# Performance work log

Measured on AMD Instinct MI355X. Metric: run time of the kernel, lower is better.

The kernel has to match this reference:

```python
import jax, jax.numpy as jnp
import numpy as np

N_HEADS = 32
N_KV = 8
HEAD_DIM = 128
THETA = 1000000.0


def setup_inputs() -> dict:
    key = jax.random.key(0)
    ks = jax.random.split(key, 7)
    batch, q_len, history = 4, 1024, 1024
    T = batch * q_len
    H = N_HEADS * HEAD_DIM  # 4096
    kv_len = q_len + history
    block_size = 64
    num_blocks = batch * (kv_len // block_size)  # 128
    s = 0.02
    return {
        'hidden_states': jax.random.normal(ks[0], (T, H), jnp.float32),
        'wq': jax.random.normal(ks[1], (H, N_HEADS * HEAD_DIM), jnp.float32) * s,
        'wk': jax.random.normal(ks[2], (H, N_KV * HEAD_DIM), jnp.float32) * s,
        'wv': jax.random.normal(ks[3], (H, N_KV * HEAD_DIM), jnp.float32) * s,
        'wo': jax.random.normal(ks[4], (N_HEADS * HEAD_DIM, H), jnp.float32) * s,
        'k_cache': jax.random.normal(ks[5], (num_blocks, block_size, N_KV, HEAD_DIM), jnp.float32),
        'v_cache': jax.random.normal(ks[6], (num_blocks, block_size, N_KV, HEAD_DIM), jnp.float32),
        'q_len': q_len,
        'history': history,
        'window': 1024,
    }


def _rotate_half(x):
    d = x.shape[-1]
    return jnp.concatenate([-x[..., d // 2:], x[..., :d // 2]], axis=-1)


def reference(hidden_states, wq, wk, wv, wo, k_cache, v_cache, q_len, history, window):
    T, H = hidden_states.shape
    batch = T // q_len
    kv_len = q_len + history
    nb, bs, n_kv, d = k_cache.shape
    blocks_per_seq = kv_len // bs
    # block table: sequence b owns contiguous blocks (paged layout)
    block_offsets = jnp.arange(batch * blocks_per_seq).reshape(batch, blocks_per_seq)

    # QKV projections
    q = (hidden_states @ wq).reshape(T, N_HEADS, d)
    k = (hidden_states @ wk).reshape(T, n_kv, d)
    v = (hidden_states @ wv).reshape(T, n_kv, d)

    # RoPE using 1d position ids (global positions of new tokens)
    pos = jnp.broadcast_to(history + jnp.arange(q_len), (batch, q_len)).reshape(T)
    inv_freq = 1.0 / (THETA ** (jnp.arange(0, d, 2, dtype=jnp.float32) / d))
    freqs = pos[:, None].astype(jnp.float32) * inv_freq[None, :]
    emb = jnp.concatenate([freqs, freqs], axis=-1)  # [T, d]
    cos = jnp.cos(emb)[:, None, :].astype(q.dtype)
    sin = jnp.sin(emb)[:, None, :].astype(q.dtype)
    q = q * cos + _rotate_half(q) * sin
    k = k * cos + _rotate_half(k) * sin

    # fill_kv_cache: scatter new K/V into paged slots history..kv_len-1
    new_pos = history + jnp.arange(q_len)  # [q_len]
    slot = (block_offsets[:, new_pos // bs] * bs + new_pos % bs).reshape(T)
    k_flat = k_cache.reshape(nb * bs, n_kv, d).at[slot].set(k)
    v_flat = v_cache.reshape(nb * bs, n_kv, d).at[slot].set(v)

    # paged gather of the full KV window per sequence
    all_pos = jnp.arange(kv_len)
    gslot = block_offsets[:, all_pos // bs] * bs + all_pos % bs  # [batch, kv_len]
    k_all = k_flat[gslot]  # [batch, kv_len, n_kv, d]
    v_all = v_flat[gslot]

    # GQA: expand kv heads
    rep = N_HEADS // n_kv
    k_all = jnp.repeat(k_all, rep, axis=2)
    v_all = jnp.repeat(v_all, rep, axis=2)

    qb = q.reshape(batch, q_len, N_HEADS, d)
    scores = jnp.einsum('bqhd,bkhd->bhqk', qb, k_all) / jnp.sqrt(jnp.asarray(d, qb.dtype))

    # causal + sliding-window mask on global positions
    qpos = history + jnp.arange(q_len)
    kpos = jnp.arange(kv_len)
    mask = kpos[None, :] <= qpos[:, None]
    if window > 0:
        mask = mask & ((qpos[:, None] - kpos[None, :]) < window)
    neg = jnp.finfo(scores.dtype).min
    scores = jnp.where(mask[None, None], scores, neg)
    attn = jax.nn.softmax(scores, axis=-1)
    out = jnp.einsum('bhqk,bkhd->bqhd', attn, v_all).reshape(T, N_HEADS * d)
    return out @ wo
```

## Files before the change

kernel.cpp:

```cpp
#include <hip/hip_runtime.h>
#include <hip/hip_bf16.h>

typedef __bf16 bf16x8 __attribute__((ext_vector_type(8)));
typedef __bf16 bf16x4 __attribute__((ext_vector_type(4)));
typedef float  f32x4  __attribute__((ext_vector_type(4)));

#define QL 1024
#define NH 32
#define NKV 8
#define HD 128
#define KVLEN 2048
#define QKV_LD 6144

typedef const __attribute__((address_space(1))) void gv_t;
typedef __attribute__((address_space(3))) void lv_t;
__device__ __forceinline__ void gll16(const void* g, void* l) {
  __builtin_amdgcn_global_load_lds((gv_t*)g, (lv_t*)l, 16, 0, 0);
}

__global__ __launch_bounds__(256) void cast_plain(const float* __restrict__ in,
                                                  __bf16* __restrict__ out, int n4) {
  int i = blockIdx.x * 256 + threadIdx.x;
  if (i >= n4) return;
  float4 v = ((const float4*)in)[i];
  bf16x4 o;
  o[0] = (__bf16)v.x; o[1] = (__bf16)v.y; o[2] = (__bf16)v.z; o[3] = (__bf16)v.w;
  ((bf16x4*)out)[i] = o;
}

__global__ __launch_bounds__(256) void transpose_cast(const float* __restrict__ in,
                                                      __bf16* __restrict__ out,
                                                      int R, int C) {
  __shared__ __bf16 tile[64][65];
  int r0 = blockIdx.y * 64, c0 = blockIdx.x * 64;
  int t = threadIdx.x;
  int tr = t >> 4, tc = (t & 15) * 4;
#pragma unroll
  for (int pass = 0; pass < 4; pass++) {
    int r = pass * 16 + tr;
    float4 v = *(const float4*)(in + (size_t)(r0 + r) * C + c0 + tc);
    tile[r][tc + 0] = (__bf16)v.x;
    tile[r][tc + 1] = (__bf16)v.y;
    tile[r][tc + 2] = (__bf16)v.z;
    tile[r][tc + 3] = (__bf16)v.w;
  }
  __syncthreads();
#pragma unroll
  for (int pass = 0; pass < 4; pass++) {
    int cc = pass * 16 + tr;
    bf16x4 o;
#pragma unroll
    for (int j = 0; j < 4; j++) o[j] = tile[tc + j][cc];
    *(bf16x4*)(out + (size_t)(c0 + cc) * R + r0 + tc) = o;
  }
}

template <int OUT_BF16>
__global__ __launch_bounds__(512, 2) void gemm256(const __bf16* __restrict__ A,
                                                  const __bf16* __restrict__ Bt,
                                                  void* __restrict__ Cout,
                                                  int M, int N, int K) {
  __shared__ __attribute__((aligned(16))) __bf16 sA[4][8192];
  __shared__ __attribute__((aligned(16))) __bf16 sB[4][8192];
  const int tid = threadIdx.x;
  const int lane = tid & 63;
  const int wave = tid >> 6;
  const int wm = wave >> 2, wn = wave & 3;
  const int quad = lane >> 4, l16 = lane & 15;

  const int nwg = gridDim.x;
  const int id = blockIdx.x;
  const int swz = (id & 7) * (nwg >> 3) + (id >> 3);
  const int gx = N >> 8;
  const int by = swz / gx, bx = swz - by * gx;
  const int row0 = by * 256, col0 = bx * 256;

  const int qsel = (tid & 3) ^ ((tid >> 3) & 3);
  const __bf16* pA0 = A + (size_t)(row0 + (tid >> 2)) * K + qsel * 8;
  const __bf16* pA1 = pA0 + (size_t)128 * K;
  const __bf16* pB0 = Bt + (size_t)(col0 + (tid >> 2)) * K + qsel * 8;
  const __bf16* pB1 = pB0 + (size_t)128 * K;

  const int xsw = (l16 >> 1) & 3;
  const int aoff = (wm * 128 + l16) * 32 + (quad ^ xsw) * 8;
  const int boff = (wn * 64 + l16) * 32 + (quad ^ xsw) * 8;

  f32x4 acc[8][4];
#pragma unroll
  for (int mt = 0; mt < 8; mt++)
#pragma unroll
    for (int nt = 0; nt < 4; nt++) acc[mt][nt] = (f32x4){0.f, 0.f, 0.f, 0.f};

  const int nT = K >> 5;

  for (int pt = 0; pt < 3; ++pt) {
    __bf16* dA = &sA[pt][0];
    __bf16* dB = &sB[pt][0];
    gll16(pA0, dA + tid * 8);
    gll16(pA1, dA + 4096 + tid * 8);
    gll16(pB0, dB + tid * 8);
    gll16(pB1, dB + 4096 + tid * 8);
    pA0 += 32; pA1 += 32; pB0 += 32; pB1 += 32;
  }
  asm volatile("s_waitcnt vmcnt(8)" ::: "memory");
  __builtin_amdgcn_s_barrier();

  for (int t = 0; t < nT; ++t) {
    const int bt = t & 3;
    const bool st = (t + 3 < nT);
    const __bf16* Ab = &sA[bt][aoff];
    const __bf16* Bb = &sB[bt][boff];
    __bf16* dA = &sA[(t + 3) & 3][0];
    __bf16* dB = &sB[(t + 3) & 3][0];
    bf16x8 a[4], b[4];

#pragma unroll
    for (int i = 0; i < 4; ++i) a[i] = *(const bf16x8*)(Ab + i * 512);
#pragma unroll
    for (int i = 0; i < 4; ++i) b[i] = *(const bf16x8*)(Bb + i * 512);
    if (st) {
      gll16(pA0, dA + tid * 8);
      gll16(pA1, dA + 4096 + tid * 8);
    }
    asm volatile("" ::: "memory");
    __builtin_amdgcn_s_barrier();
    __builtin_amdgcn_s_setprio(1);
#pragma unroll
    for (int mt = 0; mt < 4; ++mt)
#pragma unroll
      for (int nt = 0; nt < 4; ++nt)
        acc[mt][nt] = __builtin_amdgcn_mfma_f32_16x16x32_bf16(a[mt], b[nt], acc[mt][nt], 0, 0, 0);
    __builtin_amdgcn_s_setprio(0);
    __builtin_amdgcn_s_barrier();

#pragma unroll
    for (int i = 0; i < 4; ++i) a[i] = *(const bf16x8*)(Ab + (4 + i) * 512);
    if (st) {
      gll16(pB0, dB + tid * 8);
      gll16(pB1, dB + 4096 + tid * 8);
      pA0 += 32; pA1 += 32; pB0 += 32; pB1 += 32;
    }
    if (t + 3 < nT) {
      asm volatile("s_waitcnt vmcnt(8)" ::: "memory");
    } else if (t + 2 < nT) {
      asm volatile("s_waitcnt vmcnt(4)" ::: "memory");
    } else if (t + 1 < nT) {
      asm volatile("s_waitcnt vmcnt(0)" ::: "memory");
    }
    __builtin_amdgcn_s_barrier();
    __builtin_amdgcn_s_setprio(1);
#pragma unroll
    for (int mt = 0; mt < 4; ++mt)
#pragma unroll
      for (int nt = 0; nt < 4; ++nt)
        acc[4 + mt][nt] = __builtin_amdgcn_mfma_f32_16x16x32_bf16(a[mt], b[nt], acc[4 + mt][nt], 0, 0, 0);
    __builtin_amdgcn_s_setprio(0);
    __builtin_amdgcn_s_barrier();
  }

#pragma unroll
  for (int mt = 0; mt < 8; ++mt) {
#pragma unroll
    for (int r = 0; r < 4; ++r) {
      const int grow = row0 + wm * 128 + mt * 16 + quad * 4 + r;
#pragma unroll
      for (int nt = 0; nt < 4; ++nt) {
        const int gcol = col0 + wn * 64 + nt * 16 + l16;
        float v = acc[mt][nt][r];
        if (OUT_BF16)
          ((__bf16*)Cout)[(size_t)grow * N + gcol] = (__bf16)v;
        else
          ((float*)Cout)[(size_t)grow * N + gcol] = v;
      }
    }
  }
}

__global__ __launch_bounds__(256) void rope_kernel(__bf16* __restrict__ qkv) {
  int idx = blockIdx.x * 256 + threadIdx.x;
  int m = idx & 63;
  int rest = idx >> 6;
  int t = rest / 40;
  int head = rest - t * 40;
  int i = t & (QL - 1);
  float pos = (float)(1024 + i);
  float ang = pos * exp2f(-(float)m * 0.31143075889569403f);
  float c = cosf(ang), sn = sinf(ang);
  size_t base = (size_t)t * QKV_LD + head * HD;
  float x0 = (float)qkv[base + m];
  float x1 = (float)qkv[base + 64 + m];
  qkv[base + m]      = (__bf16)(x0 * c - x1 * sn);
  qkv[base + 64 + m] = (__bf16)(x1 * c + x0 * sn);
}

__global__ __launch_bounds__(256) void kv_build_k(const float* __restrict__ kcache,
                                                  const __bf16* __restrict__ qkv,
                                                  __bf16* __restrict__ k_all) {
  int idx = blockIdx.x * 256 + threadIdx.x;
  int d8 = (idx & 15) * 8;
  int p = (idx >> 4) & (KVLEN - 1);
  int bk = idx >> 15;
  int b = bk >> 3, kvh = bk & 7;
  __bf16* dst = k_all + ((size_t)bk * KVLEN + p) * HD + d8;
  if (p < 1024) {
    const float* src = kcache + ((size_t)(b * KVLEN + p) * NKV + kvh) * HD + d8;
    bf16x8 o;
#pragma unroll
    for (int j = 0; j < 8; j++) o[j] = (__bf16)src[j];
    *(bf16x8*)dst = o;
  } else {
    const __bf16* src = qkv + (size_t)(b * QL + p - 1024) * QKV_LD + 4096 + kvh * HD + d8;
    *(bf16x8*)dst = *(const bf16x8*)src;
  }
}

__global__ __launch_bounds__(256) void kv_build_vT(const float* __restrict__ vcache,
                                                   const __bf16* __restrict__ qkv,
                                                   __bf16* __restrict__ v_allT) {
  __shared__ __bf16 tile[64][130];
  int blk = blockIdx.x;
  int pt = blk & 31, bk = blk >> 5;
  int b = bk >> 3, kvh = bk & 7;
  int p0 = pt * 64;
  int t = threadIdx.x;
  int lr = t >> 4, d8 = (t & 15) * 8;
#pragma unroll
  for (int pass = 0; pass < 4; pass++) {
    int pl = pass * 16 + lr;
    int p = p0 + pl;
    if (p < 1024) {
      const float* src = vcache + ((size_t)(b * KVLEN + p) * NKV + kvh) * HD + d8;
#pragma unroll
      for (int j = 0; j < 8; j++) tile[pl][d8 + j] = (__bf16)src[j];
    } else {
      const __bf16* src = qkv + (size_t)(b * QL + p - 1024) * QKV_LD + 5120 + kvh * HD + d8;
      bf16x8 v = *(const bf16x8*)src;
#pragma unroll
      for (int j = 0; j < 8; j++) tile[pl][d8 + j] = v[j];
    }
  }
  __syncthreads();
#pragma unroll
  for (int pass = 0; pass < 4; pass++) {
    int d = (t >> 3) + pass * 32;
    int ps = (t & 7) * 8;
    bf16x8 o;
#pragma unroll
    for (int j = 0; j < 8; j++) o[j] = tile[ps + j][d];
    *(bf16x8*)(v_allT + ((size_t)bk * HD + d) * KVLEN + p0 + ps) = o;
  }
}

__global__ __launch_bounds__(256) void attn_kernel(const __bf16* __restrict__ qkv,
                                                   const __bf16* __restrict__ k_all,
                                                   const __bf16* __restrict__ v_allT,
                                                   __bf16* __restrict__ out) {
  __shared__ __attribute__((aligned(16))) __bf16 sK[64 * 128];
  __shared__ __attribute__((aligned(16))) __bf16 sV[128 * 64];
  __shared__ __attribute__((aligned(16))) __bf16 sP[4][32 * 72];
  const int tid = threadIdx.x;
  const int lane = tid & 63;
  const int wave = tid >> 6;
  const int quad = lane >> 4, l16 = lane & 15;
  const int bid = blockIdx.x;
  const int b = bid & 3;
  const int kvh = (bid >> 2) & 7;
  const int qt = bid >> 5;
  const int h = kvh * 4 + wave;
  const int i0 = qt * 32;

  const __bf16* kb = k_all + (size_t)(b * NKV + kvh) * KVLEN * HD;
  const __bf16* vb = v_allT + (size_t)(b * NKV + kvh) * HD * KVLEN;

  bf16x8 qf[2][4];
#pragma unroll
  for (int mt = 0; mt < 2; mt++) {
    const __bf16* qb = qkv + (size_t)(b * QL + i0 + mt * 16 + l16) * QKV_LD + h * HD + quad * 8;
#pragma unroll
    for (int kc = 0; kc < 4; kc++) qf[mt][kc] = *(const bf16x8*)(qb + kc * 32);
  }

  int kgo[4], vgo[4];
#pragma unroll
  for (int j = 0; j < 4; j++) {
    int g = wave * 4 + j;
    kgo[j] = (g * 4 + quad) * HD + (l16 ^ (g & 7)) * 8;
    int d = g * 8 + (lane >> 3);
    vgo[j] = d * KVLEN + ((lane & 7) ^ ((lane >> 3) & 7)) * 8;
  }
  __bf16* kls = sK + (wave * 4) * 512 + lane * 8;
  __bf16* vls = sV + (wave * 4) * 512 + lane * 8;

  f32x4 o[8][2];
#pragma unroll
  for (int dt = 0; dt < 8; dt++)
#pragma unroll
    for (int mt = 0; mt < 2; mt++) o[dt][mt] = (f32x4){0.f, 0.f, 0.f, 0.f};
  f32x4 lac[2];
  lac[0] = (f32x4){0.f, 0.f, 0.f, 0.f};
  lac[1] = (f32x4){0.f, 0.f, 0.f, 0.f};

  bf16x8 ones;
#pragma unroll
  for (int j = 0; j < 8; j++) ones[j] = (__bf16)1.0f;

  __bf16* myP = &sP[wave][0];
  const float ES = 0.12751744f;

  const int cs = (i0 + 1) & ~63;
  const int xsw = l16 & 7;

#pragma unroll
  for (int j = 0; j < 4; j++) gll16(kb + (size_t)cs * HD + kgo[j], kls + j * 512);
#pragma unroll
  for (int j = 0; j < 4; j++) gll16(vb + (size_t)cs + vgo[j], vls + j * 512);

  for (int ci = 0; ci < 17; ci++) {
    const int c = cs + ci * 64;
    __syncthreads();
    f32x4 s[2][4];
#pragma unroll
    for (int nt = 0; nt < 4; nt++) {
      s[0][nt] = (f32x4){0.f, 0.f, 0.f, 0.f};
      s[1][nt] = (f32x4){0.f, 0.f, 0.f, 0.f};
      const __bf16* kp = sK + (4 * l16 + nt) * HD;
#pragma unroll
      for (int kc = 0; kc < 4; kc++) {
        bf16x8 kf = *(const bf16x8*)(kp + ((4 * kc + quad) ^ xsw) * 8);
        s[0][nt] = __builtin_amdgcn_mfma_f32_16x16x32_bf16(qf[0][kc], kf, s[0][nt], 0, 0, 0);
        s[1][nt] = __builtin_amdgcn_mfma_f32_16x16x32_bf16(qf[1][kc], kf, s[1][nt], 0, 0, 0);
      }
    }
    __syncthreads();
    if (ci < 16) {
#pragma unroll
      for (int j = 0; j < 4; j++) gll16(kb + (size_t)(c + 64) * HD + kgo[j], kls + j * 512);
    }
    const bool full = (c >= i0 + 32) && (c <= i0 + 961);
#pragma unroll
    for (int mt = 0; mt < 2; mt++) {
#pragma unroll
      for (int r = 0; r < 4; r++) {
        bf16x4 pk;
        if (full) {
#pragma unroll
          for (int nt = 0; nt < 4; nt++) pk[nt] = (__bf16)exp2f(s[mt][nt][r] * ES);
        } else {
          const int irow = i0 + mt * 16 + quad * 4 + r;
#pragma unroll
          for (int nt = 0; nt < 4; nt++) {
            const int kk = c + 4 * l16 + nt;
            const bool valid = (kk > irow) && (kk <= irow + 1024);
            pk[nt] = valid ? (__bf16)exp2f(s[mt][nt][r] * ES) : (__bf16)0.0f;
          }
        }
        *(bf16x4*)(myP + (mt * 16 + quad * 4 + r) * 72 + 4 * l16) = pk;
      }
    }
    asm volatile("s_waitcnt lgkmcnt(0)" ::: "memory");
#pragma unroll
    for (int kc = 0; kc < 2; kc++) {
      bf16x8 pf0 = *(const bf16x8*)(myP + (l16) * 72 + kc * 32 + quad * 8);
      bf16x8 pf1 = *(const bf16x8*)(myP + (16 + l16) * 72 + kc * 32 + quad * 8);
      lac[0] = __builtin_amdgcn_mfma_f32_16x16x32_bf16(pf0, ones, lac[0], 0, 0, 0);
      lac[1] = __builtin_amdgcn_mfma_f32_16x16x32_bf16(pf1, ones, lac[1], 0, 0, 0);
#pragma unroll
      for (int dt = 0; dt < 8; dt++) {
        bf16x8 vf = *(const bf16x8*)(sV + (dt * 16 + l16) * 64 + ((kc * 4 + quad) ^ xsw) * 8);
        o[dt][0] = __builtin_amdgcn_mfma_f32_16x16x32_bf16(pf0, vf, o[dt][0], 0, 0, 0);
        o[dt][1] = __builtin_amdgcn_mfma_f32_16x16x32_bf16(pf1, vf, o[dt][1], 0, 0, 0);
      }
    }
    __syncthreads();
    if (ci < 16) {
#pragma unroll
      for (int j = 0; j < 4; j++) gll16(vb + (size_t)(c + 64) + vgo[j], vls + j * 512);
    }
  }

  float inv[2][4];
#pragma unroll
  for (int mt = 0; mt < 2; mt++)
#pragma unroll
    for (int r = 0; r < 4; r++) inv[mt][r] = 1.0f / lac[mt][r];
#pragma unroll
  for (int dt = 0; dt < 8; dt++)
#pragma unroll
    for (int mt = 0; mt < 2; mt++)
#pragma unroll
      for (int r = 0; r < 4; r++)
        out[(size_t)(b * QL + i0 + mt * 16 + quad * 4 + r) * (NH * HD) + h * HD + dt * 16 + l16] =
            (__bf16)(o[dt][mt][r] * inv[mt][r]);
}

extern "C" void kernel_launch(void* const* d_in, const int* in_sizes, int n_in,
                              void* d_out, int out_size, void* d_ws, size_t ws_size,
                              hipStream_t stream) {
  const float* hidden = (const float*)d_in[0];
  const float* wq = (const float*)d_in[1];
  const float* wk = (const float*)d_in[2];
  const float* wv = (const float*)d_in[3];
  const float* wo = (const float*)d_in[4];
  const float* kcache = (const float*)d_in[5];
  const float* vcache = (const float*)d_in[6];
  (void)in_sizes; (void)n_in; (void)out_size; (void)ws_size;

  char* w = (char*)d_ws;
  __bf16* hid_b  = (__bf16*)(w);
  __bf16* wqkvT  = (__bf16*)(w + 33554432ULL);
  __bf16* qkv    = (__bf16*)(w + 83886080ULL);
  __bf16* k_all  = (__bf16*)(w + 134217728ULL);
  __bf16* v_allT = (__bf16*)(w + 150994944ULL);
  __bf16* attn   = hid_b;
  __bf16* woT    = wqkvT;

  cast_plain<<<16384, 256, 0, stream>>>(hidden, hid_b, 4194304);
  transpose_cast<<<dim3(64, 64), 256, 0, stream>>>(wq, wqkvT, 4096, 4096);
  transpose_cast<<<dim3(16, 64), 256, 0, stream>>>(wk, wqkvT + 16777216ULL, 4096, 1024);
  transpose_cast<<<dim3(16, 64), 256, 0, stream>>>(wv, wqkvT + 20971520ULL, 4096, 1024);
  gemm256<1><<<dim3(384), 512, 0, stream>>>(hid_b, wqkvT, (void*)qkv, 4096, 6144, 4096);
  rope_kernel<<<40960, 256, 0, stream>>>(qkv);
  kv_build_k<<<4096, 256, 0, stream>>>(kcache, qkv, k_all);
  kv_build_vT<<<1024, 256, 0, stream>>>(vcache, qkv, v_allT);
  attn_kernel<<<1024, 256, 0, stream>>>(qkv, k_all, v_allT, attn);
  transpose_cast<<<dim3(64, 64), 256, 0, stream>>>(wo, woT, 4096, 4096);
  gemm256<0><<<dim3(256), 512, 0, stream>>>(attn, woT, d_out, 4096, 4096, 4096);
}
```

Measured before the change: 773.9 us.

## Switch GEMMs to 128x256 tiles with double-buffered 64-wide K stages

Replaces the 256x256 GEMM tile with a 128x256 tile using 64-wide K steps split into two halves, double-buffered in LDS instead of a 4-deep 32-wide ring. It doubles the grid (768 and 512 workgroups) to fill more of the 256 CUs and better balance the tail wave. It also adds serpentine ordering of column tiles on odd rows for L2 reuse. The trade-offs are lower arithmetic intensity per tile and a shallower prefetch pipeline.

```diff
diff --git a/kernel.cpp b/kernel.cpp
--- a/kernel.cpp
+++ b/kernel.cpp
@@ -56,12 +56,12 @@
 }
 
 template <int OUT_BF16>
-__global__ __launch_bounds__(512, 2) void gemm256(const __bf16* __restrict__ A,
-                                                  const __bf16* __restrict__ Bt,
-                                                  void* __restrict__ Cout,
-                                                  int M, int N, int K) {
-  __shared__ __attribute__((aligned(16))) __bf16 sA[4][8192];
-  __shared__ __attribute__((aligned(16))) __bf16 sB[4][8192];
+__global__ __launch_bounds__(512, 2) void gemm128x256(const __bf16* __restrict__ A,
+                                                      const __bf16* __restrict__ Bt,
+                                                      void* __restrict__ Cout,
+                                                      int M, int N, int K) {
+  __shared__ __attribute__((aligned(16))) __bf16 sA[2][8192];
+  __shared__ __attribute__((aligned(16))) __bf16 sB[2][16384];
   const int tid = threadIdx.x;
   const int lane = tid & 63;
   const int wave = tid >> 6;
@@ -70,82 +70,80 @@
 
   const int nwg = gridDim.x;
   const int id = blockIdx.x;
-  const int swz = (id & 7) * (nwg >> 3) + (id >> 3);
+  int swz = (id & 7) * (nwg >> 3) + (id >> 3);
   const int gx = N >> 8;
-  const int by = swz / gx, bx = swz - by * gx;
-  const int row0 = by * 256, col0 = bx * 256;
+  int by = swz / gx;
+  int bx = swz - by * gx;
+  if (by & 1) bx = gx - 1 - bx;
+  const int row0 = by * 128, col0 = bx * 256;
 
   const int qsel = (tid & 3) ^ ((tid >> 3) & 3);
-  const __bf16* pA0 = A + (size_t)(row0 + (tid >> 2)) * K + qsel * 8;
-  const __bf16* pA1 = pA0 + (size_t)128 * K;
-  const __bf16* pB0 = Bt + (size_t)(col0 + (tid >> 2)) * K + qsel * 8;
-  const __bf16* pB1 = pB0 + (size_t)128 * K;
-
-  const int xsw = (l16 >> 1) & 3;
-  const int aoff = (wm * 128 + l16) * 32 + (quad ^ xsw) * 8;
-  const int boff = (wn * 64 + l16) * 32 + (quad ^ xsw) * 8;
-
-  f32x4 acc[8][4];
-#pragma unroll
-  for (int mt = 0; mt < 8; mt++)
+  const __bf16* gA  = A  + (size_t)(row0 + (tid >> 2)) * K + qsel * 8;
+  const __bf16* gB0 = Bt + (size_t)(col0 + (tid >> 2)) * K + qsel * 8;
+  const __bf16* gB1 = gB0 + (size_t)128 * K;
+
+  const int xq = (quad ^ ((l16 >> 1) & 3)) * 8;
+  const int abase = (wm * 64 + l16) * 32 + xq;
+  const int bbase = (wn * 64 + l16) * 32 + xq;
+
+  f32x4 acc[4][4];
+#pragma unroll
+  for (int mt = 0; mt < 4; mt++)
 #pragma unroll
     for (int nt = 0; nt < 4; nt++) acc[mt][nt] = (f32x4){0.f, 0.f, 0.f, 0.f};
 
-  const int nT = K >> 5;
-
-  for (int pt = 0; pt < 3; ++pt) {
-    __bf16* dA = &sA[pt][0];
-    __bf16* dB = &sB[pt][0];
-    gll16(pA0, dA + tid * 8);
-    gll16(pA1, dA + 4096 + tid * 8);
-    gll16(pB0, dB + tid * 8);
-    gll16(pB1, dB + 4096 + tid * 8);
-    pA0 += 32; pA1 += 32; pB0 += 32; pB1 += 32;
-  }
-  asm volatile("s_waitcnt vmcnt(8)" ::: "memory");
+  const int nT = K >> 6;
+
+#define STAGE_A(t_, kh_)                                                        \
+  gll16(gA + (size_t)(t_)*64 + (kh_)*32, &sA[(t_) & 1][(kh_)*4096] + tid * 8)
+#define STAGE_B(t_, kh_)                                                        \
+  do {                                                                          \
+    __bf16* d_ = &sB[(t_) & 1][(kh_)*8192];                                     \
+    gll16(gB0 + (size_t)(t_)*64 + (kh_)*32, d_ + tid * 8);                      \
+    gll16(gB1 + (size_t)(t_)*64 + (kh_)*32, d_ + 4096 + tid * 8);               \
+  } while (0)
+
+  STAGE_A(0, 0); STAGE_B(0, 0);
+  STAGE_A(0, 1); STAGE_B(0, 1);
+  if (nT > 1) { STAGE_A(1, 0); STAGE_B(1, 0); }
+  asm volatile("s_waitcnt vmcnt(6)" ::: "memory");
   __builtin_amdgcn_s_barrier();
 
   for (int t = 0; t < nT; ++t) {
-    const int bt = t & 3;
-    const bool st = (t + 3 < nT);
-    const __bf16* Ab = &sA[bt][aoff];
-    const __bf16* Bb = &sB[bt][boff];
-    __bf16* dA = &sA[(t + 3) & 3][0];
-    __bf16* dB = &sB[(t + 3) & 3][0];
-    bf16x8 a[4], b[4];
-
-#pragma unroll
-    for (int i = 0; i < 4; ++i) a[i] = *(const bf16x8*)(Ab + i * 512);
-#pragma unroll
-    for (int i = 0; i < 4; ++i) b[i] = *(const bf16x8*)(Bb + i * 512);
-    if (st) {
-      gll16(pA0, dA + tid * 8);
-      gll16(pA1, dA + 4096 + tid * 8);
-    }
-    asm volatile("" ::: "memory");
+    const __bf16* Ab = &sA[t & 1][0];
+    const __bf16* Bb = &sB[t & 1][0];
+    bf16x8 af[4], bfr[4];
+
+#pragma unroll
+    for (int i = 0; i < 4; ++i) af[i]  = *(const bf16x8*)(Ab + abase + i * 512);
+#pragma unroll
+    for (int i = 0; i < 4; ++i) bfr[i] = *(const bf16x8*)(Bb + bbase + i * 512);
+    if (t + 1 < nT) {
+      STAGE_A(t + 1, 1); STAGE_B(t + 1, 1);
+      asm volatile("s_waitcnt vmcnt(6)" ::: "memory");
+    } else {
+      asm volatile("s_waitcnt vmcnt(0)" ::: "memory");
+    }
     __builtin_amdgcn_s_barrier();
     __builtin_amdgcn_s_setprio(1);
 #pragma unroll
     for (int mt = 0; mt < 4; ++mt)
 #pragma unroll
       for (int nt = 0; nt < 4; ++nt)
-        acc[mt][nt] = __builtin_amdgcn_mfma_f32_16x16x32_bf16(a[mt], b[nt], acc[mt][nt], 0, 0, 0);
+        acc[mt][nt] = __builtin_amdgcn_mfma_f32_16x16x32_bf16(af[mt], bfr[nt], acc[mt][nt], 0, 0, 0);
     __builtin_amdgcn_s_setprio(0);
-    __builtin_amdgcn_s_barrier();
-
-#pragma unroll
-    for (int i = 0; i < 4; ++i) a[i] = *(const bf16x8*)(Ab + (4 + i) * 512);
-    if (st) {
-      gll16(pB0, dB + tid * 8);
-      gll16(pB1, dB + 4096 + tid * 8);
-      pA0 += 32; pA1 += 32; pB0 += 32; pB1 += 32;
-    }
-    if (t + 3 < nT) {
-      asm volatile("s_waitcnt vmcnt(8)" ::: "memory");
-    } else if (t + 2 < nT) {
-      asm volatile("s_waitcnt vmcnt(4)" ::: "memory");
+
+#pragma unroll
+    for (int i = 0; i < 4; ++i) af[i]  = *(const bf16x8*)(Ab + 4096 + abase + i * 512);
+#pragma unroll
+    for (int i = 0; i < 4; ++i) bfr[i] = *(const bf16x8*)(Bb + 8192 + bbase + i * 512);
+    if (t + 2 < nT) {
+      STAGE_A(t + 2, 0); STAGE_B(t + 2, 0);
+      asm volatile("s_waitcnt vmcnt(6)" ::: "memory");
     } else if (t + 1 < nT) {
-      asm volatile("s_waitcnt vmcnt(0)" ::: "memory");
+      asm volatile("s_waitcnt vmcnt(3)" ::: "memory");
+    } else {
+      asm volatile("" ::: "memory");
     }
     __builtin_amdgcn_s_barrier();
     __builtin_amdgcn_s_setprio(1);
@@ -153,16 +151,17 @@
     for (int mt = 0; mt < 4; ++mt)
 #pragma unroll
       for (int nt = 0; nt < 4; ++nt)
-        acc[4 + mt][nt] = __builtin_amdgcn_mfma_f32_16x16x32_bf16(a[mt], b[nt], acc[4 + mt][nt], 0, 0, 0);
+        acc[mt][nt] = __builtin_amdgcn_mfma_f32_16x16x32_bf16(af[mt], bfr[nt], acc[mt][nt], 0, 0, 0);
     __builtin_amdgcn_s_setprio(0);
-    __builtin_amdgcn_s_barrier();
-  }
-
-#pragma unroll
-  for (int mt = 0; mt < 8; ++mt) {
+  }
+#undef STAGE_A
+#undef STAGE_B
+
+#pragma unroll
+  for (int mt = 0; mt < 4; ++mt) {
 #pragma unroll
     for (int r = 0; r < 4; ++r) {
-      const int grow = row0 + wm * 128 + mt * 16 + quad * 4 + r;
+      const int grow = row0 + wm * 64 + mt * 16 + quad * 4 + r;
 #pragma unroll
       for (int nt = 0; nt < 4; ++nt) {
         const int gcol = col0 + wn * 64 + nt * 16 + l16;
@@ -418,11 +417,11 @@
   transpose_cast<<<dim3(64, 64), 256, 0, stream>>>(wq, wqkvT, 4096, 4096);
   transpose_cast<<<dim3(16, 64), 256, 0, stream>>>(wk, wqkvT + 16777216ULL, 4096, 1024);
   transpose_cast<<<dim3(16, 64), 256, 0, stream>>>(wv, wqkvT + 20971520ULL, 4096, 1024);
-  gemm256<1><<<dim3(384), 512, 0, stream>>>(hid_b, wqkvT, (void*)qkv, 4096, 6144, 4096);
+  gemm128x256<1><<<dim3(768), 512, 0, stream>>>(hid_b, wqkvT, (void*)qkv, 4096, 6144, 4096);
   rope_kernel<<<40960, 256, 0, stream>>>(qkv);
   kv_build_k<<<4096, 256, 0, stream>>>(kcache, qkv, k_all);
   kv_build_vT<<<1024, 256, 0, stream>>>(vcache, qkv, v_allT);
   attn_kernel<<<1024, 256, 0, stream>>>(qkv, k_all, v_allT, attn);
   transpose_cast<<<dim3(64, 64), 256, 0, stream>>>(wo, woT, 4096, 4096);
-  gemm256<0><<<dim3(256), 512, 0, stream>>>(attn, woT, d_out, 4096, 4096, 4096);
-}
+  gemm128x256<0><<<dim3(512), 512, 0, stream>>>(attn, woT, d_out, 4096, 4096, 4096);
+}
```

Measured after the change: 802.9 us. 3.7% more time.

## Add 128x256-tile GEMM for QKV projection and restructure RoPE per token

Applied to the files above, without the earlier changes.

Adds a new bf16 MFMA GEMM kernel with 128x256 tiles, double-buffered LDS staging through global_load_lds, an XOR-swizzled LDS layout, priority hints, and launch bounds that allow two blocks per CU. The QKV projection switches to it with 768 workgroups instead of 384, aiming for more waves on the device and better tail balance. The RoPE kernel now gives one block per token and loops over the 40 heads, so cos/sin are computed once per thread rather than once per element. The cost is less reuse per tile, since each block covers half as many rows as before.

```diff
diff --git a/kernel.cpp b/kernel.cpp
--- a/kernel.cpp
+++ b/kernel.cpp
@@ -176,21 +176,145 @@
   }
 }
 
+template <int OUT_BF16>
+__global__ __launch_bounds__(512, 2) void gemm128x256(const __bf16* __restrict__ A,
+                                                      const __bf16* __restrict__ Bt,
+                                                      void* __restrict__ Cout,
+                                                      int M, int N, int K) {
+  __shared__ __attribute__((aligned(16))) __bf16 sA[2][8192];
+  __shared__ __attribute__((aligned(16))) __bf16 sB[2][16384];
+  const int tid = threadIdx.x;
+  const int lane = tid & 63;
+  const int wave = tid >> 6;
+  const int wm = wave >> 2, wn = wave & 3;
+  const int quad = lane >> 4, l16 = lane & 15;
+
+  const int nwg = gridDim.x;
+  const int id = blockIdx.x;
+  int swz = (id & 7) * (nwg >> 3) + (id >> 3);
+  const int gx = N >> 8;
+  int by = swz / gx;
+  int bx = swz - by * gx;
+  if (by & 1) bx = gx - 1 - bx;
+  const int row0 = by * 128, col0 = bx * 256;
+
+  const int qsel = (tid & 3) ^ ((tid >> 3) & 3);
+  const __bf16* gA  = A  + (size_t)(row0 + (tid >> 2)) * K + qsel * 8;
+  const __bf16* gB0 = Bt + (size_t)(col0 + (tid >> 2)) * K + qsel * 8;
+  const __bf16* gB1 = gB0 + (size_t)128 * K;
+
+  const int xq = (quad ^ ((l16 >> 1) & 3)) * 8;
+  const int abase = (wm * 64 + l16) * 32 + xq;
+  const int bbase = (wn * 64 + l16) * 32 + xq;
+
+  f32x4 acc[4][4];
+#pragma unroll
+  for (int mt = 0; mt < 4; mt++)
+#pragma unroll
+    for (int nt = 0; nt < 4; nt++) acc[mt][nt] = (f32x4){0.f, 0.f, 0.f, 0.f};
+
+  const int nT = K >> 6;
+
+#define STAGE_A(t_, kh_)                                                        \
+  gll16(gA + (size_t)(t_)*64 + (kh_)*32, &sA[(t_) & 1][(kh_)*4096] + tid * 8)
+#define STAGE_B(t_, kh_)                                                        \
+  do {                                                                          \
+    __bf16* d_ = &sB[(t_) & 1][(kh_)*8192];                                     \
+    gll16(gB0 + (size_t)(t_)*64 + (kh_)*32, d_ + tid * 8);                      \
+    gll16(gB1 + (size_t)(t_)*64 + (kh_)*32, d_ + 4096 + tid * 8);               \
+  } while (0)
+
+  STAGE_A(0, 0); STAGE_B(0, 0);
+  STAGE_A(0, 1); STAGE_B(0, 1);
+  if (nT > 1) { STAGE_A(1, 0); STAGE_B(1, 0); }
+  asm volatile("s_waitcnt vmcnt(6)" ::: "memory");
+  __builtin_amdgcn_s_barrier();
+
+  for (int t = 0; t < nT; ++t) {
+    const __bf16* Ab = &sA[t & 1][0];
+    const __bf16* Bb = &sB[t & 1][0];
+    bf16x8 af[4], bfr[4];
+
+#pragma unroll
+    for (int i = 0; i < 4; ++i) af[i]  = *(const bf16x8*)(Ab + abase + i * 512);
+#pragma unroll
+    for (int i = 0; i < 4; ++i) bfr[i] = *(const bf16x8*)(Bb + bbase + i * 512);
+    if (t + 1 < nT) {
+      STAGE_A(t + 1, 1); STAGE_B(t + 1, 1);
+      asm volatile("s_waitcnt vmcnt(6)" ::: "memory");
+    } else {
+      asm volatile("s_waitcnt vmcnt(0)" ::: "memory");
+    }
+    __builtin_amdgcn_s_barrier();
+    __builtin_amdgcn_s_setprio(1);
+#pragma unroll
+    for (int mt = 0; mt < 4; ++mt)
+#pragma unroll
+      for (int nt = 0; nt < 4; ++nt)
+        acc[mt][nt] = __builtin_amdgcn_mfma_f32_16x16x32_bf16(af[mt], bfr[nt], acc[mt][nt], 0, 0, 0);
+    __builtin_amdgcn_s_setprio(0);
+
+#pragma unroll
+    for (int i = 0; i < 4; ++i) af[i]  = *(const bf16x8*)(Ab + 4096 + abase + i * 512);
+#pragma unroll
+    for (int i = 0; i < 4; ++i) bfr[i] = *(const bf16x8*)(Bb + 8192 + bbase + i * 512);
+    if (t + 2 < nT) {
+      STAGE_A(t + 2, 0); STAGE_B(t + 2, 0);
+      asm volatile("s_waitcnt vmcnt(6)" ::: "memory");
+    } else if (t + 1 < nT) {
+      asm volatile("s_waitcnt vmcnt(3)" ::: "memory");
+    } else {
+      asm volatile("" ::: "memory");
+    }
+    __builtin_amdgcn_s_barrier();
+    __builtin_amdgcn_s_setprio(1);
+#pragma unroll
+    for (int mt = 0; mt < 4; ++mt)
+#pragma unroll
+      for (int nt = 0; nt < 4; ++nt)
+        acc[mt][nt] = __builtin_amdgcn_mfma_f32_16x16x32_bf16(af[mt], bfr[nt], acc[mt][nt], 0, 0, 0);
+    __builtin_amdgcn_s_setprio(0);
+  }
+#undef STAGE_A
+#undef STAGE_B
+
+#pragma unroll
+  for (int mt = 0; mt < 4; ++mt) {
+#pragma unroll
+    for (int r = 0; r < 4; ++r) {
+      const int grow = row0 + wm * 64 + mt * 16 + quad * 4 + r;
+#pragma unroll
+      for (int nt = 0; nt < 4; ++nt) {
+        const int gcol = col0 + wn * 64 + nt * 16 + l16;
+        float v = acc[mt][nt][r];
+        if (OUT_BF16)
+          ((__bf16*)Cout)[(size_t)grow * N + gcol] = (__bf16)v;
+        else
+          ((float*)Cout)[(size_t)grow * N + gcol] = v;
+      }
+    }
+  }
+}
+
 __global__ __launch_bounds__(256) void rope_kernel(__bf16* __restrict__ qkv) {
-  int idx = blockIdx.x * 256 + threadIdx.x;
-  int m = idx & 63;
-  int rest = idx >> 6;
-  int t = rest / 40;
-  int head = rest - t * 40;
+  int t = blockIdx.x;
+  int tid = threadIdx.x;
+  int hg = tid >> 6;
+  int m = tid & 63;
   int i = t & (QL - 1);
   float pos = (float)(1024 + i);
   float ang = pos * exp2f(-(float)m * 0.31143075889569403f);
   float c = cosf(ang), sn = sinf(ang);
-  size_t base = (size_t)t * QKV_LD + head * HD;
-  float x0 = (float)qkv[base + m];
-  float x1 = (float)qkv[base + 64 + m];
-  qkv[base + m]      = (__bf16)(x0 * c - x1 * sn);
-  qkv[base + 64 + m] = (__bf16)(x1 * c + x0 * sn);
+  size_t row = (size_t)t * QKV_LD;
+#pragma unroll
+  for (int u = 0; u < 10; u++) {
+    int head = hg + u * 4;
+    size_t base = row + head * HD;
+    float x0 = (float)qkv[base + m];
+    float x1 = (float)qkv[base + 64 + m];
+    qkv[base + m]      = (__bf16)(x0 * c - x1 * sn);
+    qkv[base + 64 + m] = (__bf16)(x1 * c + x0 * sn);
+  }
 }
 
 __global__ __launch_bounds__(256) void kv_build_k(const float* __restrict__ kcache,
@@ -418,8 +542,8 @@
   transpose_cast<<<dim3(64, 64), 256, 0, stream>>>(wq, wqkvT, 4096, 4096);
   transpose_cast<<<dim3(16, 64), 256, 0, stream>>>(wk, wqkvT + 16777216ULL, 4096, 1024);
   transpose_cast<<<dim3(16, 64), 256, 0, stream>>>(wv, wqkvT + 20971520ULL, 4096, 1024);
-  gemm256<1><<<dim3(384), 512, 0, stream>>>(hid_b, wqkvT, (void*)qkv, 4096, 6144, 4096);
-  rope_kernel<<<40960, 256, 0, stream>>>(qkv);
+  gemm128x256<1><<<dim3(768), 512, 0, stream>>>(hid_b, wqkvT, (void*)qkv, 4096, 6144, 4096);
+  rope_kernel<<<4096, 256, 0, stream>>>(qkv);
   kv_build_k<<<4096, 256, 0, stream>>>(kcache, qkv, k_all);
   kv_build_vT<<<1024, 256, 0, stream>>>(vcache, qkv, v_allT);
   attn_kernel<<<1024, 256, 0, stream>>>(qkv, k_all, v_allT, attn);
```

Result: no change. 765.2 us (-1.1%).
